# Kernel tuning notes

Hardware: AMD Instinct MI355X
Metric: run time of the kernel (lower is better)

## Reference

```python
import jax, jax.numpy as jnp
import numpy as np

X_DIM, H_DIM, Y_DIM, ROLLOUT = 256, 2048, 256, 4096


def setup_inputs() -> dict:
    key = jax.random.key(0)
    ks = jax.random.split(key, 6)
    inp = {
        "x": jax.random.normal(ks[0], (1, ROLLOUT, X_DIM), dtype=jnp.float32),
        "h": jnp.zeros((H_DIM,), dtype=jnp.float32),
        "Wc": jax.random.normal(ks[1], (X_DIM + H_DIM, H_DIM), dtype=jnp.float32) * 0.01,
        "Wu": jax.random.normal(ks[2], (X_DIM + H_DIM, H_DIM), dtype=jnp.float32) * 0.01,
        "Wr": jax.random.normal(ks[3], (X_DIM + H_DIM, H_DIM), dtype=jnp.float32) * 0.01,
        "bc": jnp.zeros((H_DIM,), dtype=jnp.float32),
        "bu": jnp.zeros((H_DIM,), dtype=jnp.float32),
        "br": jnp.zeros((H_DIM,), dtype=jnp.float32),
        "Wh_y": jax.random.normal(ks[4], (H_DIM, Y_DIM), dtype=jnp.float32) * 0.01,
        "by": jnp.zeros((Y_DIM,), dtype=jnp.float32),
    }
    return inp


def reference(x, h, Wc, Wu, Wr, bc, bu, br, Wh_y, by):
    xs = x[0]  # [T, x_dim]

    def step(hid, xt):
        xc = jnp.concatenate([xt, hid])                      # [x_dim + h_dim]
        Lu = jax.nn.sigmoid(xc @ Wu + bu)                    # update gate
        Lr = jax.nn.sigmoid(xc @ Wr + br)                    # reset gate
        xr = jnp.concatenate([xt, hid * Lr])
        c_tilda = jnp.tanh(xr @ Wc + bc)
        h_new = c_tilda * Lu + hid * (1.0 - Lu)
        y = h_new @ Wh_y + by
        return h_new, y

    h_fin, ys = jax.lax.scan(step, h, xs)  # ys: [T, y_dim]
    return ys, h_fin
```

## Files before the change

kernel.cpp:

```cpp
#include <hip/hip_runtime.h>
#include <hip/hip_bf16.h>

#define TSTEPS 4096
#define XD 256
#define HD 2048
#define YD 256
#define KD 2304
#define NWG 256
#define NT 512

#define WU_OFF 0
#define WR_OFF (8*KD*2)
#define WC_OFF (16*KD*2)
#define WY_OFF (24*KD*2)
#define HBUF_OFF (WY_OFF + HD*4)
#define ZBUF_OFF (HBUF_OFF + HD*4)
#define RED_OFF (ZBUF_OFF + HD*4)
#define LDS_BYTES (RED_OFF + 256)

#define HFLAGS_U32 0
#define RFLAGS_U32 8192
#define HGO_U32    16384
#define RGO_U32    18432
#define WS_ZERO_BYTES 81920
#define HB0_OFF 81920
#define HB1_OFF 90112
#define RB0_OFF 98304
#define RB1_OFF 106496

__device__ __forceinline__ float bflo(unsigned u){ return __uint_as_float(u << 16); }
__device__ __forceinline__ float bfhi(unsigned u){ return __uint_as_float(u & 0xffff0000u); }
__device__ __forceinline__ unsigned short f2bf(float f){
  unsigned b = __float_as_uint(f);
  b += 0x7fffu + ((b >> 16) & 1u);
  return (unsigned short)(b >> 16);
}
__device__ __forceinline__ float sigmoidf_(float x){ return 1.0f / (1.0f + __expf(-x)); }

__device__ __forceinline__ void gst32f(float* p, float v){
  __hip_atomic_store(p, v, __ATOMIC_RELAXED, __HIP_MEMORY_SCOPE_AGENT);
}
__device__ __forceinline__ void flagst(unsigned* p, unsigned v){
  __hip_atomic_store(p, v, __ATOMIC_RELAXED, __HIP_MEMORY_SCOPE_AGENT);
}
__device__ __forceinline__ void spinflag(const unsigned* p, unsigned epoch, long* budget){
  while (__hip_atomic_load(p, __ATOMIC_RELAXED, __HIP_MEMORY_SCOPE_AGENT) < epoch) {
    if (--(*budget) < 0) break;
    __builtin_amdgcn_s_sleep(1);
  }
}

__device__ __forceinline__ float4 cohload16(const float4* p){
  float4 r;
  asm volatile("global_load_dwordx4 %0, %1, off sc1\n\t"
               "s_waitcnt vmcnt(0)"
               : "=v"(r) : "v"(p) : "memory");
  return r;
}
__device__ __forceinline__ float4 cohload16_issue(const float4* p){
  float4 r;
  asm volatile("global_load_dwordx4 %0, %1, off sc1"
               : "=v"(r) : "v"(p) : "memory");
  return r;
}

__device__ __forceinline__ void hub_wait(unsigned* flags, unsigned* go,
                                         unsigned epoch, int tid, long* budget){
  if (tid >= 1 && tid < NWG) spinflag(flags + tid*32, epoch, budget);
  __syncthreads();
  if (tid < 64) flagst(go + tid*32, epoch);
}
__device__ __forceinline__ void wave_wait(unsigned* go, unsigned epoch,
                                          int line, int l6, long* budget){
  if (l6 == 0) spinflag(go + line*32, epoch, budget);
}

template<int I0, int I1, int STRIDE>
__device__ __forceinline__ void dotacc(const float* v, const unsigned short* wcol,
                                       int lane, float4& acc){
  #pragma unroll
  for (int i = I0; i < I1; ++i) {
    int k = 4 * (lane + STRIDE * i);
    float4 vv = *(const float4*)(v + k);
    uint2  wq = *(const uint2*)(wcol + k);
    acc.x = fmaf(vv.x, bflo(wq.x), acc.x);
    acc.y = fmaf(vv.y, bfhi(wq.x), acc.y);
    acc.z = fmaf(vv.z, bflo(wq.y), acc.z);
    acc.w = fmaf(vv.w, bfhi(wq.y), acc.w);
  }
}

__device__ __forceinline__ void xpart(const float4 xq, const unsigned short* wcol,
                                      int l6, float4& acc){
  uint2 wq = *(const uint2*)(wcol + 4*l6);
  acc.x = fmaf(xq.x, bflo(wq.x), acc.x);
  acc.y = fmaf(xq.y, bfhi(wq.x), acc.y);
  acc.z = fmaf(xq.z, bflo(wq.y), acc.z);
  acc.w = fmaf(xq.w, bfhi(wq.y), acc.w);
}

__device__ __forceinline__ float redux64(float4 a){
  float s = (a.x + a.y) + (a.z + a.w);
  s += __shfl_xor(s, 32); s += __shfl_xor(s, 16); s += __shfl_xor(s, 8);
  s += __shfl_xor(s, 4);  s += __shfl_xor(s, 2);  s += __shfl_xor(s, 1);
  return s;
}

extern "C" __global__ void __launch_bounds__(NT)
gru_persistent(const float* __restrict__ x,  const float* __restrict__ h0,
               const float* __restrict__ Wc, const float* __restrict__ Wu,
               const float* __restrict__ Wr, const float* __restrict__ bc,
               const float* __restrict__ bu, const float* __restrict__ br,
               const float* __restrict__ Wy, const float* __restrict__ by,
               float* __restrict__ out, unsigned* wsu)
{
  extern __shared__ char smem[];
  unsigned short* wuS = (unsigned short*)(smem + WU_OFF);
  unsigned short* wrS = (unsigned short*)(smem + WR_OFF);
  unsigned short* wcS = (unsigned short*)(smem + WC_OFF);
  float* wyS   = (float*)(smem + WY_OFF);
  float* hbufS = (float*)(smem + HBUF_OFF);
  float* zbufS = (float*)(smem + ZBUF_OFF);
  float* red   = (float*)(smem + RED_OFF);

  unsigned* hflags = wsu + HFLAGS_U32;
  unsigned* rflags = wsu + RFLAGS_U32;
  unsigned* hgo    = wsu + HGO_U32;
  unsigned* rgo    = wsu + RGO_U32;
  float* hb[2] = { (float*)((char*)wsu + HB0_OFF), (float*)((char*)wsu + HB1_OFF) };
  float* rb[2] = { (float*)((char*)wsu + RB0_OFF), (float*)((char*)wsu + RB1_OFF) };

  const int wg = blockIdx.x, tid = threadIdx.x;
  const int col0 = 8 * wg;

  for (int idx = tid; idx < 8*KD; idx += NT) {
    int c = idx & 7, k = idx >> 3;
    size_t g = (size_t)k * HD + col0 + c;
    wuS[c*KD + k] = f2bf(Wu[g]);
    wrS[c*KD + k] = f2bf(Wr[g]);
    wcS[c*KD + k] = f2bf(Wc[g]);
  }
  for (int k = tid; k < HD; k += NT) wyS[k] = Wy[(size_t)k * YD + wg];
  if (tid < 8) {
    red[16+tid] = bu[col0+tid];
    red[24+tid] = br[col0+tid];
    red[32+tid] = bc[col0+tid];
  }
  if (tid == 0) red[40] = by[wg];
  __syncthreads();

  long budget = 20000000;

  const int w  = tid >> 6, l6 = tid & 63;
  const int goline = ((wg & 7) << 3) + w;
  const unsigned short* ucol = wuS + w * KD;
  const unsigned short* rcol = wrS + w * KD;
  const unsigned short* ccol = wcS + w * KD;

  float4 xq = ((const float4*)x)[l6];
  float ureg = 0.f;

  auto window = [&](int t){
    float4 au = make_float4(0.f, 0.f, 0.f, 0.f);
    xpart(xq, ucol, l6, au);
    dotacc<1, 9, 64>(hbufS - XD, ucol, l6, au);
    ureg = sigmoidf_(redux64(au) + red[16 + w]);
    int k = 256 * w + 4 * l6;
    float4 hv4 = *(const float4*)(hbufS + k);
    float4 wy4 = *(const float4*)(wyS + k);
    float ys = fmaf(hv4.x, wy4.x, fmaf(hv4.y, wy4.y, fmaf(hv4.z, wy4.z, hv4.w * wy4.w)));
    ys += __shfl_xor(ys, 32); ys += __shfl_xor(ys, 16); ys += __shfl_xor(ys, 8);
    ys += __shfl_xor(ys, 4);  ys += __shfl_xor(ys, 2);  ys += __shfl_xor(ys, 1);
    if (l6 == 0) red[8 + w] = ys;
    if (t + 1 < TSTEPS) xq = ((const float4*)(x + (size_t)(t+1) * XD))[l6];
  };

  for (int t = 0; t < TSTEPS; ++t) {
    float4 a1 = make_float4(0.f, 0.f, 0.f, 0.f);
    xpart(xq, rcol, l6, a1);

    if (t == 0) {
      ((float4*)hbufS)[tid] = ((const float4*)h0)[tid];
    } else {
      if (wg == 0) hub_wait(hflags, hgo, (unsigned)t, tid, &budget);
      else         wave_wait(hgo, (unsigned)t, goline, l6, &budget);
      float4 hv = cohload16((const float4*)hb[(t+1)&1] + tid);
      ((float4*)hbufS)[tid] = hv;
    }
    __syncthreads();

    dotacc<1, 9, 64>(hbufS - XD, rcol, l6, a1);
    {
      float s = redux64(a1);
      if (l6 == 0)
        gst32f(rb[t&1] + col0 + w,
               sigmoidf_(s + red[24 + w]) * hbufS[col0 + w]);
    }
    __syncthreads();
    if (tid == 0) flagst(rflags + wg*32, (unsigned)(t+1));

    float4 a2 = make_float4(0.f, 0.f, 0.f, 0.f);
    xpart(xq, ccol, l6, a2);

    float4 rv;
    if (wg != 0) {
      window(t);
      wave_wait(rgo, (unsigned)(t+1), goline, l6, &budget);
      rv = cohload16((const float4*)rb[t&1] + tid);
    } else {
      hub_wait(rflags, rgo, (unsigned)(t+1), tid, &budget);
      rv = cohload16_issue((const float4*)rb[t&1] + tid);
      window(t);
      asm volatile("s_waitcnt vmcnt(0)" ::: "memory");
    }
    ((float4*)zbufS)[tid] = rv;
    __syncthreads();

    if (tid == 0 && t > 0) {
      float y = red[8]+red[9]+red[10]+red[11]+red[12]+red[13]+red[14]+red[15] + red[40];
      out[(size_t)(t-1) * YD + wg] = y;
    }

    dotacc<1, 9, 64>(zbufS - XD, ccol, l6, a2);
    {
      float s = redux64(a2);
      if (l6 == 0) {
        float cc = tanhf(s + red[32 + w]);
        float hp = hbufS[col0 + w];
        gst32f(hb[t&1] + col0 + w, cc * ureg + hp * (1.0f - ureg));
      }
    }
    __syncthreads();
    if (tid == 0) flagst(hflags + wg*32, (unsigned)(t+1));
  }

  if (wg == 0) hub_wait(hflags, hgo, (unsigned)TSTEPS, tid, &budget);
  else         wave_wait(hgo, (unsigned)TSTEPS, goline, l6, &budget);
  {
    float4 hv = cohload16((const float4*)hb[(TSTEPS-1)&1] + tid);
    ((float4*)hbufS)[tid] = hv;
  }
  __syncthreads();
  {
    int k = 256 * w + 4 * l6;
    float4 hv4 = *(const float4*)(hbufS + k);
    float4 wy4 = *(const float4*)(wyS + k);
    float ys = fmaf(hv4.x, wy4.x, fmaf(hv4.y, wy4.y, fmaf(hv4.z, wy4.z, hv4.w * wy4.w)));
    ys += __shfl_xor(ys, 32); ys += __shfl_xor(ys, 16); ys += __shfl_xor(ys, 8);
    ys += __shfl_xor(ys, 4);  ys += __shfl_xor(ys, 2);  ys += __shfl_xor(ys, 1);
    if (l6 == 0) red[8 + w] = ys;
  }
  __syncthreads();
  if (tid == 0) {
    float y = red[8]+red[9]+red[10]+red[11]+red[12]+red[13]+red[14]+red[15] + red[40];
    out[(size_t)(TSTEPS-1) * YD + wg] = y;
  }
  if (tid < 8) out[(size_t)TSTEPS * YD + col0 + tid] = hbufS[col0 + tid];
}

extern "C" void kernel_launch(void* const* d_in, const int* in_sizes, int n_in,
                              void* d_out, int out_size, void* d_ws, size_t ws_size,
                              hipStream_t stream) {
  const float* x  = (const float*)d_in[0];
  const float* h0 = (const float*)d_in[1];
  const float* Wc = (const float*)d_in[2];
  const float* Wu = (const float*)d_in[3];
  const float* Wr = (const float*)d_in[4];
  const float* bc = (const float*)d_in[5];
  const float* bu = (const float*)d_in[6];
  const float* br = (const float*)d_in[7];
  const float* Wy = (const float*)d_in[8];
  const float* by = (const float*)d_in[9];
  float* out = (float*)d_out;
  unsigned* wsu = (unsigned*)d_ws;

  hipFuncSetAttribute((const void*)gru_persistent,
                      hipFuncAttributeMaxDynamicSharedMemorySize, LDS_BYTES);
  hipMemsetAsync(d_ws, 0, WS_ZERO_BYTES, stream);
  gru_persistent<<<dim3(NWG), dim3(NT), LDS_BYTES, stream>>>(
      x, h0, Wc, Wu, Wr, bc, bu, br, Wy, by, out, wsu);
}
```

Baseline: 21.17 ms.

## Replace per-workgroup flags with tag bits embedded in published state values

Each published h and r value now carries a 2-bit step tag in its low mantissa bits. The hub workgroup polls the data buffers directly until every tag matches, instead of waiting on 256 per-workgroup flags. The other workgroups still spin on eight go lines, but only thread 0 spins, followed by a block barrier. This removes the flag store, the extra barrier after each publish, and a round of flag traffic per phase. It also keeps each workgroup's own h slice in LDS rather than re-reading it. The cost is a loss of two mantissa bits of precision in h and r, and slower repeated polling of the full 8KB buffer by the hub.

```diff
diff --git a/kernel.cpp b/kernel.cpp
--- a/kernel.cpp
+++ b/kernel.cpp
@@ -18,15 +18,13 @@
 #define RED_OFF (ZBUF_OFF + HD*4)
 #define LDS_BYTES (RED_OFF + 256)
 
-#define HFLAGS_U32 0
-#define RFLAGS_U32 8192
-#define HGO_U32    16384
-#define RGO_U32    18432
-#define WS_ZERO_BYTES 81920
-#define HB0_OFF 81920
-#define HB1_OFF 90112
-#define RB0_OFF 98304
-#define RB1_OFF 106496
+#define HGO_U32 0
+#define RGO_U32 256
+#define WS_ZERO_BYTES 34816
+#define HB0_OFF 2048
+#define HB1_OFF 10240
+#define RB0_OFF 18432
+#define RB1_OFF 26624
 
 __device__ __forceinline__ float bflo(unsigned u){ return __uint_as_float(u << 16); }
 __device__ __forceinline__ float bfhi(unsigned u){ return __uint_as_float(u & 0xffff0000u); }
@@ -37,8 +35,9 @@
 }
 __device__ __forceinline__ float sigmoidf_(float x){ return 1.0f / (1.0f + __expf(-x)); }
 
-__device__ __forceinline__ void gst32f(float* p, float v){
-  __hip_atomic_store(p, v, __ATOMIC_RELAXED, __HIP_MEMORY_SCOPE_AGENT);
+__device__ __forceinline__ void storetag(float* p, float v, unsigned tag){
+  unsigned b = (__float_as_uint(v) & ~3u) | tag;
+  __hip_atomic_store((unsigned*)p, b, __ATOMIC_RELAXED, __HIP_MEMORY_SCOPE_AGENT);
 }
 __device__ __forceinline__ void flagst(unsigned* p, unsigned v){
   __hip_atomic_store(p, v, __ATOMIC_RELAXED, __HIP_MEMORY_SCOPE_AGENT);
@@ -46,6 +45,20 @@
 __device__ __forceinline__ void spinflag(const unsigned* p, unsigned epoch, long* budget){
   while (__hip_atomic_load(p, __ATOMIC_RELAXED, __HIP_MEMORY_SCOPE_AGENT) < epoch) {
     if (--(*budget) < 0) break;
+    __builtin_amdgcn_s_sleep(1);
+  }
+}
+
+__device__ __forceinline__ float4 pollchunk16(const float4* p, unsigned tag, long* budget){
+  for (;;) {
+    float4 r;
+    asm volatile("global_load_dwordx4 %0, %1, off sc1\n\t"
+                 "s_waitcnt vmcnt(0)"
+                 : "=v"(r) : "v"(p) : "memory");
+    unsigned m = (__float_as_uint(r.x)^tag) | (__float_as_uint(r.y)^tag)
+               | (__float_as_uint(r.z)^tag) | (__float_as_uint(r.w)^tag);
+    if ((m & 3u) == 0u) return r;
+    if (--(*budget) < 0) return r;
     __builtin_amdgcn_s_sleep(1);
   }
 }
@@ -56,23 +69,6 @@
                "s_waitcnt vmcnt(0)"
                : "=v"(r) : "v"(p) : "memory");
   return r;
-}
-__device__ __forceinline__ float4 cohload16_issue(const float4* p){
-  float4 r;
-  asm volatile("global_load_dwordx4 %0, %1, off sc1"
-               : "=v"(r) : "v"(p) : "memory");
-  return r;
-}
-
-__device__ __forceinline__ void hub_wait(unsigned* flags, unsigned* go,
-                                         unsigned epoch, int tid, long* budget){
-  if (tid >= 1 && tid < NWG) spinflag(flags + tid*32, epoch, budget);
-  __syncthreads();
-  if (tid < 64) flagst(go + tid*32, epoch);
-}
-__device__ __forceinline__ void wave_wait(unsigned* go, unsigned epoch,
-                                          int line, int l6, long* budget){
-  if (l6 == 0) spinflag(go + line*32, epoch, budget);
 }
 
 template<int I0, int I1, int STRIDE>
@@ -89,7 +85,6 @@
     acc.w = fmaf(vv.w, bfhi(wq.y), acc.w);
   }
 }
-
 __device__ __forceinline__ void xpart(const float4 xq, const unsigned short* wcol,
                                       int l6, float4& acc){
   uint2 wq = *(const uint2*)(wcol + 4*l6);
@@ -98,7 +93,6 @@
   acc.z = fmaf(xq.z, bflo(wq.y), acc.z);
   acc.w = fmaf(xq.w, bfhi(wq.y), acc.w);
 }
-
 __device__ __forceinline__ float redux64(float4 a){
   float s = (a.x + a.y) + (a.z + a.w);
   s += __shfl_xor(s, 32); s += __shfl_xor(s, 16); s += __shfl_xor(s, 8);
@@ -123,10 +117,8 @@
   float* zbufS = (float*)(smem + ZBUF_OFF);
   float* red   = (float*)(smem + RED_OFF);
 
-  unsigned* hflags = wsu + HFLAGS_U32;
-  unsigned* rflags = wsu + RFLAGS_U32;
-  unsigned* hgo    = wsu + HGO_U32;
-  unsigned* rgo    = wsu + RGO_U32;
+  unsigned* hgo = wsu + HGO_U32;
+  unsigned* rgo = wsu + RGO_U32;
   float* hb[2] = { (float*)((char*)wsu + HB0_OFF), (float*)((char*)wsu + HB1_OFF) };
   float* rb[2] = { (float*)((char*)wsu + RB0_OFF), (float*)((char*)wsu + RB1_OFF) };
 
@@ -145,6 +137,7 @@
     red[16+tid] = bu[col0+tid];
     red[24+tid] = br[col0+tid];
     red[32+tid] = bc[col0+tid];
+    red[56+tid] = h0[col0+tid];
   }
   if (tid == 0) red[40] = by[wg];
   __syncthreads();
@@ -152,7 +145,6 @@
   long budget = 20000000;
 
   const int w  = tid >> 6, l6 = tid & 63;
-  const int goline = ((wg & 7) << 3) + w;
   const unsigned short* ucol = wuS + w * KD;
   const unsigned short* rcol = wrS + w * KD;
   const unsigned short* ccol = wcS + w * KD;
@@ -181,11 +173,16 @@
 
     if (t == 0) {
       ((float4*)hbufS)[tid] = ((const float4*)h0)[tid];
+    } else if (wg == 0) {
+      float4 hv = pollchunk16((const float4*)hb[(t+1)&1] + tid,
+                              (unsigned)(t & 3), &budget);
+      __syncthreads();
+      if (tid < 8) flagst(hgo + tid*32, (unsigned)t);
+      ((float4*)hbufS)[tid] = hv;
     } else {
-      if (wg == 0) hub_wait(hflags, hgo, (unsigned)t, tid, &budget);
-      else         wave_wait(hgo, (unsigned)t, goline, l6, &budget);
-      float4 hv = cohload16((const float4*)hb[(t+1)&1] + tid);
-      ((float4*)hbufS)[tid] = hv;
+      if (tid == 0) spinflag(hgo + (wg & 7)*32, (unsigned)t, &budget);
+      __syncthreads();
+      ((float4*)hbufS)[tid] = cohload16((const float4*)hb[(t+1)&1] + tid);
     }
     __syncthreads();
 
@@ -193,27 +190,27 @@
     {
       float s = redux64(a1);
       if (l6 == 0)
-        gst32f(rb[t&1] + col0 + w,
-               sigmoidf_(s + red[24 + w]) * hbufS[col0 + w]);
-    }
-    __syncthreads();
-    if (tid == 0) flagst(rflags + wg*32, (unsigned)(t+1));
+        storetag(rb[t&1] + col0 + w,
+                 sigmoidf_(s + red[24 + w]) * red[56 + w],
+                 (unsigned)((t+1) & 3));
+    }
 
     float4 a2 = make_float4(0.f, 0.f, 0.f, 0.f);
     xpart(xq, ccol, l6, a2);
 
-    float4 rv;
-    if (wg != 0) {
+    if (wg == 0) {
+      float4 zv = pollchunk16((const float4*)rb[t&1] + tid,
+                              (unsigned)((t+1) & 3), &budget);
+      __syncthreads();
+      if (tid < 8) flagst(rgo + tid*32, (unsigned)(t+1));
+      ((float4*)zbufS)[tid] = zv;
       window(t);
-      wave_wait(rgo, (unsigned)(t+1), goline, l6, &budget);
-      rv = cohload16((const float4*)rb[t&1] + tid);
     } else {
-      hub_wait(rflags, rgo, (unsigned)(t+1), tid, &budget);
-      rv = cohload16_issue((const float4*)rb[t&1] + tid);
       window(t);
-      asm volatile("s_waitcnt vmcnt(0)" ::: "memory");
-    }
-    ((float4*)zbufS)[tid] = rv;
+      if (tid == 0) spinflag(rgo + (wg & 7)*32, (unsigned)(t+1), &budget);
+      __syncthreads();
+      ((float4*)zbufS)[tid] = cohload16((const float4*)rb[t&1] + tid);
+    }
     __syncthreads();
 
     if (tid == 0 && t > 0) {
@@ -226,19 +223,24 @@
       float s = redux64(a2);
       if (l6 == 0) {
         float cc = tanhf(s + red[32 + w]);
-        float hp = hbufS[col0 + w];
-        gst32f(hb[t&1] + col0 + w, cc * ureg + hp * (1.0f - ureg));
+        float hp = red[56 + w];
+        float hn = cc * ureg + hp * (1.0f - ureg);
+        red[56 + w] = hn;
+        storetag(hb[t&1] + col0 + w, hn, (unsigned)((t+1) & 3));
       }
     }
-    __syncthreads();
-    if (tid == 0) flagst(hflags + wg*32, (unsigned)(t+1));
-  }
-
-  if (wg == 0) hub_wait(hflags, hgo, (unsigned)TSTEPS, tid, &budget);
-  else         wave_wait(hgo, (unsigned)TSTEPS, goline, l6, &budget);
-  {
-    float4 hv = cohload16((const float4*)hb[(TSTEPS-1)&1] + tid);
+  }
+
+  if (wg == 0) {
+    float4 hv = pollchunk16((const float4*)hb[(TSTEPS-1)&1] + tid,
+                            (unsigned)(TSTEPS & 3), &budget);
+    __syncthreads();
+    if (tid < 8) flagst(hgo + tid*32, (unsigned)TSTEPS);
     ((float4*)hbufS)[tid] = hv;
+  } else {
+    if (tid == 0) spinflag(hgo + (wg & 7)*32, (unsigned)TSTEPS, &budget);
+    __syncthreads();
+    ((float4*)hbufS)[tid] = cohload16((const float4*)hb[(TSTEPS-1)&1] + tid);
   }
   __syncthreads();
   {
@@ -255,7 +257,7 @@
     float y = red[8]+red[9]+red[10]+red[11]+red[12]+red[13]+red[14]+red[15] + red[40];
     out[(size_t)(TSTEPS-1) * YD + wg] = y;
   }
-  if (tid < 8) out[(size_t)TSTEPS * YD + col0 + tid] = hbufS[col0 + tid];
+  if (tid < 8) out[(size_t)TSTEPS * YD + col0 + tid] = red[56 + tid];
 }
 
 extern "C" void kernel_launch(void* const* d_in, const int* in_sizes, int n_in,
@@ -274,9 +276,9 @@
   float* out = (float*)d_out;
   unsigned* wsu = (unsigned*)d_ws;
 
-  hipFuncSetAttribute((const void*)gru_persistent,
-                      hipFuncAttributeMaxDynamicSharedMemorySize, LDS_BYTES);
-  hipMemsetAsync(d_ws, 0, WS_ZERO_BYTES, stream);
+  (void)hipFuncSetAttribute((const void*)gru_persistent,
+                            hipFuncAttributeMaxDynamicSharedMemorySize, LDS_BYTES);
+  (void)hipMemsetAsync(d_ws, 0, WS_ZERO_BYTES, stream);
   gru_persistent<<<dim3(NWG), dim3(NT), LDS_BYTES, stream>>>(
       x, h0, Wc, Wu, Wr, bc, bu, br, Wy, by, out, wsu);
 }
```

Result: slower. 23.07 ms (+8.9%).

## Pack arrival flags densely and poll them with one wave in the hub block

Applied to the files above, without the earlier changes.

Arrival flags change from one per 128-byte line to packed contiguous words, so one wave in block 0 can poll all 256 flags with vector loads and a wave-wide all-check. This replaces the old scheme where 255 threads each spun on their own line. Spinning now keeps two coherent loads in flight so a flag change is seen sooner. The go flags are also packed at 32-byte stride. Packing flags into shared cache lines may add contention between the blocks writing them, in exchange for fewer polling loads and lower barrier latency on every timestep.

```diff
diff --git a/kernel.cpp b/kernel.cpp
--- a/kernel.cpp
+++ b/kernel.cpp
@@ -19,14 +19,14 @@
 #define LDS_BYTES (RED_OFF + 256)
 
 #define HFLAGS_U32 0
-#define RFLAGS_U32 8192
-#define HGO_U32    16384
-#define RGO_U32    18432
-#define WS_ZERO_BYTES 81920
-#define HB0_OFF 81920
-#define HB1_OFF 90112
-#define RB0_OFF 98304
-#define RB1_OFF 106496
+#define ZFLAGS_U32 512
+#define HGO_U32    1024
+#define ZGO_U32    1536
+#define WS_ZERO_BYTES 8192
+#define HB0_OFF 8192
+#define HB1_OFF 16384
+#define RB0_OFF 24576
+#define RB1_OFF 32768
 
 __device__ __forceinline__ float bflo(unsigned u){ return __uint_as_float(u << 16); }
 __device__ __forceinline__ float bfhi(unsigned u){ return __uint_as_float(u & 0xffff0000u); }
@@ -43,11 +43,56 @@
 __device__ __forceinline__ void flagst(unsigned* p, unsigned v){
   __hip_atomic_store(p, v, __ATOMIC_RELAXED, __HIP_MEMORY_SCOPE_AGENT);
 }
-__device__ __forceinline__ void spinflag(const unsigned* p, unsigned epoch, long* budget){
-  while (__hip_atomic_load(p, __ATOMIC_RELAXED, __HIP_MEMORY_SCOPE_AGENT) < epoch) {
-    if (--(*budget) < 0) break;
+
+__device__ __forceinline__ void spinflag2(const unsigned* p, unsigned epoch, long* budget){
+  unsigned a, b;
+  asm volatile("global_load_dword %0, %1, off sc1" : "=v"(a) : "v"(p) : "memory");
+  asm volatile("global_load_dword %0, %1, off sc1" : "=v"(b) : "v"(p) : "memory");
+  for (;;) {
+    asm volatile("s_waitcnt vmcnt(1)" ::: "memory");
+    __builtin_amdgcn_sched_barrier(0);
+    if (a >= epoch) break;
+    asm volatile("global_load_dword %0, %1, off sc1" : "=v"(a) : "v"(p) : "memory");
+    asm volatile("s_waitcnt vmcnt(1)" ::: "memory");
+    __builtin_amdgcn_sched_barrier(0);
+    if (b >= epoch) break;
+    asm volatile("global_load_dword %0, %1, off sc1" : "=v"(b) : "v"(p) : "memory");
+    if ((*budget -= 2) < 0) break;
     __builtin_amdgcn_s_sleep(1);
   }
+  asm volatile("s_waitcnt vmcnt(0)" ::: "memory");
+  asm volatile("" :: "v"(a), "v"(b));
+}
+
+__device__ __forceinline__ void gangpoll(const unsigned* flags, unsigned epoch,
+                                         int l6, long* budget){
+  const float4* p = (const float4*)flags + l6;
+  float4 A, B;
+  asm volatile("global_load_dwordx4 %0, %1, off sc1" : "=v"(A) : "v"(p) : "memory");
+  asm volatile("global_load_dwordx4 %0, %1, off sc1" : "=v"(B) : "v"(p) : "memory");
+  for (;;) {
+    asm volatile("s_waitcnt vmcnt(1)" ::: "memory");
+    __builtin_amdgcn_sched_barrier(0);
+    {
+      int ok = (__float_as_uint(A.x) >= epoch) & (__float_as_uint(A.y) >= epoch)
+             & (__float_as_uint(A.z) >= epoch) & (__float_as_uint(A.w) >= epoch);
+      if (__all(ok)) break;
+    }
+    asm volatile("global_load_dwordx4 %0, %1, off sc1" : "=v"(A) : "v"(p) : "memory");
+    asm volatile("s_waitcnt vmcnt(1)" ::: "memory");
+    __builtin_amdgcn_sched_barrier(0);
+    {
+      int ok = (__float_as_uint(B.x) >= epoch) & (__float_as_uint(B.y) >= epoch)
+             & (__float_as_uint(B.z) >= epoch) & (__float_as_uint(B.w) >= epoch);
+      if (__all(ok)) break;
+    }
+    asm volatile("global_load_dwordx4 %0, %1, off sc1" : "=v"(B) : "v"(p) : "memory");
+    if ((*budget -= 2) < 0) break;
+    __builtin_amdgcn_s_sleep(1);
+  }
+  asm volatile("s_waitcnt vmcnt(0)" ::: "memory");
+  asm volatile("" :: "v"(A.x), "v"(A.y), "v"(A.z), "v"(A.w),
+                     "v"(B.x), "v"(B.y), "v"(B.z), "v"(B.w));
 }
 
 __device__ __forceinline__ float4 cohload16(const float4* p){
@@ -62,17 +107,6 @@
   asm volatile("global_load_dwordx4 %0, %1, off sc1"
                : "=v"(r) : "v"(p) : "memory");
   return r;
-}
-
-__device__ __forceinline__ void hub_wait(unsigned* flags, unsigned* go,
-                                         unsigned epoch, int tid, long* budget){
-  if (tid >= 1 && tid < NWG) spinflag(flags + tid*32, epoch, budget);
-  __syncthreads();
-  if (tid < 64) flagst(go + tid*32, epoch);
-}
-__device__ __forceinline__ void wave_wait(unsigned* go, unsigned epoch,
-                                          int line, int l6, long* budget){
-  if (l6 == 0) spinflag(go + line*32, epoch, budget);
 }
 
 template<int I0, int I1, int STRIDE>
@@ -89,7 +123,6 @@
     acc.w = fmaf(vv.w, bfhi(wq.y), acc.w);
   }
 }
-
 __device__ __forceinline__ void xpart(const float4 xq, const unsigned short* wcol,
                                       int l6, float4& acc){
   uint2 wq = *(const uint2*)(wcol + 4*l6);
@@ -98,7 +131,6 @@
   acc.z = fmaf(xq.z, bflo(wq.y), acc.z);
   acc.w = fmaf(xq.w, bfhi(wq.y), acc.w);
 }
-
 __device__ __forceinline__ float redux64(float4 a){
   float s = (a.x + a.y) + (a.z + a.w);
   s += __shfl_xor(s, 32); s += __shfl_xor(s, 16); s += __shfl_xor(s, 8);
@@ -124,9 +156,9 @@
   float* red   = (float*)(smem + RED_OFF);
 
   unsigned* hflags = wsu + HFLAGS_U32;
-  unsigned* rflags = wsu + RFLAGS_U32;
+  unsigned* zflags = wsu + ZFLAGS_U32;
   unsigned* hgo    = wsu + HGO_U32;
-  unsigned* rgo    = wsu + RGO_U32;
+  unsigned* zgo    = wsu + ZGO_U32;
   float* hb[2] = { (float*)((char*)wsu + HB0_OFF), (float*)((char*)wsu + HB1_OFF) };
   float* rb[2] = { (float*)((char*)wsu + RB0_OFF), (float*)((char*)wsu + RB1_OFF) };
 
@@ -181,11 +213,16 @@
 
     if (t == 0) {
       ((float4*)hbufS)[tid] = ((const float4*)h0)[tid];
+    } else if (wg == 0) {
+      if (w == 0) {
+        gangpoll(hflags, (unsigned)t, l6, &budget);
+        flagst(hgo + l6*8, (unsigned)t);
+      }
+      __syncthreads();
+      ((float4*)hbufS)[tid] = cohload16((const float4*)hb[(t+1)&1] + tid);
     } else {
-      if (wg == 0) hub_wait(hflags, hgo, (unsigned)t, tid, &budget);
-      else         wave_wait(hgo, (unsigned)t, goline, l6, &budget);
-      float4 hv = cohload16((const float4*)hb[(t+1)&1] + tid);
-      ((float4*)hbufS)[tid] = hv;
+      if (l6 == 0) spinflag2(hgo + goline*8, (unsigned)t, &budget);
+      ((float4*)hbufS)[tid] = cohload16((const float4*)hb[(t+1)&1] + tid);
     }
     __syncthreads();
 
@@ -197,7 +234,7 @@
                sigmoidf_(s + red[24 + w]) * hbufS[col0 + w]);
     }
     __syncthreads();
-    if (tid == 0) flagst(rflags + wg*32, (unsigned)(t+1));
+    if (tid == 0) flagst(zflags + wg, (unsigned)(t+1));
 
     float4 a2 = make_float4(0.f, 0.f, 0.f, 0.f);
     xpart(xq, ccol, l6, a2);
@@ -205,10 +242,14 @@
     float4 rv;
     if (wg != 0) {
       window(t);
-      wave_wait(rgo, (unsigned)(t+1), goline, l6, &budget);
+      if (l6 == 0) spinflag2(zgo + goline*8, (unsigned)(t+1), &budget);
       rv = cohload16((const float4*)rb[t&1] + tid);
     } else {
-      hub_wait(rflags, rgo, (unsigned)(t+1), tid, &budget);
+      if (w == 0) {
+        gangpoll(zflags, (unsigned)(t+1), l6, &budget);
+        flagst(zgo + l6*8, (unsigned)(t+1));
+      }
+      __syncthreads();
       rv = cohload16_issue((const float4*)rb[t&1] + tid);
       window(t);
       asm volatile("s_waitcnt vmcnt(0)" ::: "memory");
@@ -231,14 +272,19 @@
       }
     }
     __syncthreads();
-    if (tid == 0) flagst(hflags + wg*32, (unsigned)(t+1));
-  }
-
-  if (wg == 0) hub_wait(hflags, hgo, (unsigned)TSTEPS, tid, &budget);
-  else         wave_wait(hgo, (unsigned)TSTEPS, goline, l6, &budget);
-  {
-    float4 hv = cohload16((const float4*)hb[(TSTEPS-1)&1] + tid);
-    ((float4*)hbufS)[tid] = hv;
+    if (tid == 0) flagst(hflags + wg, (unsigned)(t+1));
+  }
+
+  if (wg == 0) {
+    if (w == 0) {
+      gangpoll(hflags, (unsigned)TSTEPS, l6, &budget);
+      flagst(hgo + l6*8, (unsigned)TSTEPS);
+    }
+    __syncthreads();
+    ((float4*)hbufS)[tid] = cohload16((const float4*)hb[(TSTEPS-1)&1] + tid);
+  } else {
+    if (l6 == 0) spinflag2(hgo + goline*8, (unsigned)TSTEPS, &budget);
+    ((float4*)hbufS)[tid] = cohload16((const float4*)hb[(TSTEPS-1)&1] + tid);
   }
   __syncthreads();
   {
@@ -274,9 +320,9 @@
   float* out = (float*)d_out;
   unsigned* wsu = (unsigned*)d_ws;
 
-  hipFuncSetAttribute((const void*)gru_persistent,
-                      hipFuncAttributeMaxDynamicSharedMemorySize, LDS_BYTES);
-  hipMemsetAsync(d_ws, 0, WS_ZERO_BYTES, stream);
+  (void)hipFuncSetAttribute((const void*)gru_persistent,
+                            hipFuncAttributeMaxDynamicSharedMemorySize, LDS_BYTES);
+  (void)hipMemsetAsync(d_ws, 0, WS_ZERO_BYTES, stream);
   gru_persistent<<<dim3(NWG), dim3(NT), LDS_BYTES, stream>>>(
       x, h0, Wc, Wu, Wr, bc, bu, br, Wy, by, out, wsu);
 }
```

New measurement: 25.99 ms. 1.23x slower.
